# Performance work log

Measured on AMD Instinct MI355X. Metric: run time of the kernel, lower is better.

The kernel has to match this reference:

```python
import jax, jax.numpy as jnp
import numpy as np

N, K, D = 200000, 16, 64


def setup_inputs() -> dict:
    key = jax.random.key(0)
    k1, k2, k3, k4 = jax.random.split(key, 4)
    X = jax.random.normal(k1, (N, D), dtype=jnp.float32)
    pi = jax.nn.softmax(jax.random.normal(k2, (K,), dtype=jnp.float32))
    mus = jax.random.normal(k3, (K, D), dtype=jnp.float32)
    # build SPD covariance matrices: A A^T + 0.5 I
    A = 0.1 * jax.random.normal(k4, (K, D, D), dtype=jnp.float32)
    covs = jnp.einsum('kij,klj->kil', A, A) + 0.5 * jnp.eye(D, dtype=jnp.float32)[None]
    return {"X": X, "pi": pi, "mus": mus, "covs": covs}


def reference(X, pi, mus, covs):
    # GaussianMixtureModel.estimate_log_prob: per-component MVN log_prob + logsumexp
    # fused into one batched Cholesky/Mahalanobis computation.
    d = X.shape[1]
    L = jnp.linalg.cholesky(covs)                      # [K, D, D]
    diff = X[None, :, :] - mus[:, None, :]             # [K, N, D]
    # solve L z = diff^T per component -> whitened residuals
    solve = jax.vmap(lambda Lk, dk: jax.scipy.linalg.solve_triangular(Lk, dk.T, lower=True))
    z = solve(L, diff)                                 # [K, D, N]
    maha = jnp.sum(z * z, axis=1)                      # [K, N]
    half_logdet = jnp.sum(jnp.log(jnp.diagonal(L, axis1=1, axis2=2)), axis=1)  # [K]
    log2pi = jnp.asarray(np.log(2.0 * np.pi), dtype=X.dtype)
    log_prob = -0.5 * (d * log2pi + maha) - half_logdet[:, None]   # [K, N]
    weighted = jnp.log(pi)[:, None] + log_prob          # [K, N]
    # stable softmax over components == exp(weighted - logsumexp)
    r_E = jax.nn.softmax(weighted, axis=0).T            # [N, K]
    return r_E
```

## Files before the change

### kernel.cpp

```cpp
#include <hip/hip_runtime.h>
#include <cstddef>
#include <cstdint>


#define GMM_D 64
#define GMM_K 16

typedef _Float16 half8 __attribute__((ext_vector_type(8)));
typedef float f32x4 __attribute__((ext_vector_type(4)));

#define WA_BYTES (GMM_K * 16 * 64 * 8 * 2)

__device__ __forceinline__ float fast_rsqrt(float x) {
#if __has_builtin(__builtin_amdgcn_rsqf)
    const float r = __builtin_amdgcn_rsqf(x);
    return r * (1.5f - 0.5f * x * r * r);
#else
    return 1.0f / sqrtf(x);
#endif
}

__device__ __forceinline__ float lane_bcast(float v, int l) {
    return __int_as_float(__builtin_amdgcn_readlane(__float_as_int(v), l));
}

__global__ __launch_bounds__(64) void gmm_precompute_kernel(
    const float* __restrict__ pi, const float* __restrict__ mus,
    const float* __restrict__ covs, _Float16* __restrict__ WA,
    float* __restrict__ tv, float* __restrict__ cc)
{
    const int k = blockIdx.x;
    const int r = threadIdx.x;

    __shared__ alignas(16) float Ls[GMM_D][68];
    __shared__ float Wv[GMM_D][GMM_D + 1];

    float A_r[GMM_D];
    {
        const float4* src = reinterpret_cast<const float4*>(
            covs + (size_t)k * GMM_D * GMM_D + (size_t)r * GMM_D);
        #pragma unroll
        for (int u = 0; u < GMM_D / 4; ++u) {
            const float4 v = src[u];
            A_r[4 * u + 0] = v.x; A_r[4 * u + 1] = v.y;
            A_r[4 * u + 2] = v.z; A_r[4 * u + 3] = v.w;
        }
    }

    float mydiag = 1.0f, myrs = 1.0f;
    #pragma unroll
    for (int j = 0; j < GMM_D; ++j) {
        const float pivot = lane_bcast(A_r[j], j);
        const float rs = fast_rsqrt(pivot);
        const float valj = A_r[j] * rs;
        if (r == j) { mydiag = valj; myrs = rs; }
        A_r[j] = valj;
        #pragma unroll
        for (int p = j + 1; p < GMM_D; ++p)
            A_r[p] -= valj * lane_bcast(valj, p);
    }

    #pragma unroll
    for (int p = 0; p < GMM_D; ++p)
        Ls[r][p] = (p <= r) ? A_r[p] : 0.0f;
    __syncthreads();

    float w[GMM_D];
    #pragma unroll
    for (int i = 0; i < GMM_D; ++i) w[i] = 0.0f;

    #pragma unroll
    for (int i = 0; i < GMM_D; ++i) {
        const f32x4* Lrow = reinterpret_cast<const f32x4*>(&Ls[i][0]);
        float a0 = 0.0f, a1 = 0.0f, a2 = 0.0f, a3 = 0.0f;
        #pragma unroll
        for (int u = 0; u <= (i >> 2); ++u) {
            const f32x4 lv = Lrow[u];
            a0 -= lv[0] * w[4 * u + 0];
            a1 -= lv[1] * w[4 * u + 1];
            a2 -= lv[2] * w[4 * u + 2];
            a3 -= lv[3] * w[4 * u + 3];
        }
        const float invd = lane_bcast(myrs, i);
        const float dlt = (r == i) ? 1.0f : 0.0f;
        w[i] = (dlt + (a0 + a1) + (a2 + a3)) * invd;
    }

    #pragma unroll
    for (int i = 0; i < GMM_D; ++i)
        Wv[i][r] = w[i];
    __syncthreads();

    {
        const float* mk = mus + k * GMM_D;
        float s0 = 0.f, s1 = 0.f, s2 = 0.f, s3 = 0.f;
        #pragma unroll
        for (int c = 0; c < GMM_D; c += 4) {
            s0 += Wv[r][c + 0] * mk[c + 0];
            s1 += Wv[r][c + 1] * mk[c + 1];
            s2 += Wv[r][c + 2] * mk[c + 2];
            s3 += Wv[r][c + 3] * mk[c + 3];
        }
        tv[k * GMM_D + r] = -((s0 + s1) + (s2 + s3));
    }

    {
        const int lr = r & 15, q = r >> 4;
        #pragma unroll
        for (int f = 0; f < 16; ++f) {
            const int mt = f >> 2, s = f & 3;
            const int row = mt * 16 + lr;
            const int db = (s & 1) * 32 + q * 8;
            half8 hv;
            #pragma unroll
            for (int u = 0; u < 8; ++u) {
                const float v = Wv[row][db + u];
                _Float16 h = (_Float16)v;
                if (s >= 2) h = (_Float16)(v - (float)h);
                hv[u] = h;
            }
            *(half8*)(WA + ((size_t)((k * 16 + f) * 64) + r) * 8) = hv;
        }
    }

    {
        float ll = logf(mydiag);
        #pragma unroll
        for (int off = 32; off > 0; off >>= 1) ll += __shfl_down(ll, off);
        if (r == 0)
            cc[k] = logf(pi[k]) - ll - 0.5f * 64.0f * 1.8378770664093453f;
    }
}

__global__ __launch_bounds__(256, 2) void gmm_estep_kernel(
    const float* __restrict__ X, const _Float16* __restrict__ WA,
    const float* __restrict__ tv, const float* __restrict__ cc,
    float* __restrict__ out, int N)
{
    __shared__ _Float16 xs[64 * 136];
    __shared__ float lg[64 * 17];

    const int tid = threadIdx.x;

    {
        const int p = tid >> 2, qq = tid & 3;
        const int np = blockIdx.x * 64 + p;
        if (np < N) {
            const float4* src = reinterpret_cast<const float4*>(X + (size_t)np * GMM_D) + qq * 4;
            float vv[16];
            #pragma unroll
            for (int u = 0; u < 4; ++u) {
                const float4 v = src[u];
                vv[4 * u + 0] = v.x; vv[4 * u + 1] = v.y;
                vv[4 * u + 2] = v.z; vv[4 * u + 3] = v.w;
            }
            half8 h0, h1, l0, l1;
            #pragma unroll
            for (int u = 0; u < 8; ++u) {
                const _Float16 a = (_Float16)vv[u];
                const _Float16 b = (_Float16)vv[u + 8];
                h0[u] = a; l0[u] = (_Float16)(vv[u] - (float)a);
                h1[u] = b; l1[u] = (_Float16)(vv[u + 8] - (float)b);
            }
            _Float16* row = xs + p * 136;
            *(half8*)(row + qq * 16)          = h0;
            *(half8*)(row + qq * 16 + 8)      = h1;
            *(half8*)(row + 64 + qq * 16)     = l0;
            *(half8*)(row + 64 + qq * 16 + 8) = l1;
        }
    }
    __syncthreads();

    const int lane = tid & 63;
    const int wave = __builtin_amdgcn_readfirstlane(tid >> 6);
    const int pt = lane & 15;
    const int q  = lane >> 4;

    #pragma unroll 1
    for (int kk = 0; kk < 4; ++kk) {
        const int k = wave * 4 + kk;

        half8 af[4][4];
        const _Float16* wab = WA + (size_t)k * 8192 + lane * 8;
        #pragma unroll
        for (int mt = 0; mt < 4; ++mt)
            #pragma unroll
            for (int s = 0; s < 4; ++s)
                af[mt][s] = *(const half8*)(wab + (mt * 4 + s) * 512);

        f32x4 tk4[4];
        #pragma unroll
        for (int mt = 0; mt < 4; ++mt)
            tk4[mt] = *(const f32x4*)(tv + k * 64 + mt * 16 + q * 4);

        #pragma unroll 1
        for (int nt = 0; nt < 4; ++nt) {
            const _Float16* xrow = xs + (nt * 16 + pt) * 136 + q * 8;
            const half8 bh0 = *(const half8*)(xrow);
            const half8 bh1 = *(const half8*)(xrow + 32);
            const half8 bl0 = *(const half8*)(xrow + 64);
            const half8 bl1 = *(const half8*)(xrow + 96);

            float mahaP = 0.0f;
            #pragma unroll
            for (int mt = 0; mt < 4; ++mt) {
                f32x4 c = tk4[mt];
                c = __builtin_amdgcn_mfma_f32_16x16x32_f16(af[mt][0], bh0, c, 0, 0, 0);
                c = __builtin_amdgcn_mfma_f32_16x16x32_f16(af[mt][1], bh1, c, 0, 0, 0);
                c = __builtin_amdgcn_mfma_f32_16x16x32_f16(af[mt][0], bl0, c, 0, 0, 0);
                c = __builtin_amdgcn_mfma_f32_16x16x32_f16(af[mt][1], bl1, c, 0, 0, 0);
                c = __builtin_amdgcn_mfma_f32_16x16x32_f16(af[mt][2], bh0, c, 0, 0, 0);
                c = __builtin_amdgcn_mfma_f32_16x16x32_f16(af[mt][3], bh1, c, 0, 0, 0);
                mahaP += c[0] * c[0] + c[1] * c[1] + c[2] * c[2] + c[3] * c[3];
            }
            mahaP += __shfl_xor(mahaP, 16);
            mahaP += __shfl_xor(mahaP, 32);
            if (q == 0 && (blockIdx.x * 64 + nt * 16 + pt) < N)
                lg[(nt * 16 + pt) * 17 + k] = cc[k] - 0.5f * mahaP;
        }
    }
    __syncthreads();

    {
        const int p = tid >> 2, qq = tid & 3;
        const int np = blockIdx.x * 64 + p;
        if (np < N) {
            const float* row = &lg[p * 17];
            float m = row[0];
            #pragma unroll
            for (int j = 1; j < GMM_K; ++j) m = fmaxf(m, row[j]);
            float e[GMM_K];
            float s = 0.0f;
            #pragma unroll
            for (int j = 0; j < GMM_K; ++j) { e[j] = __expf(row[j] - m); s += e[j]; }
            const float inv = 1.0f / s;
            float4 v;
            v.x = e[qq * 4 + 0] * inv;
            v.y = e[qq * 4 + 1] * inv;
            v.z = e[qq * 4 + 2] * inv;
            v.w = e[qq * 4 + 3] * inv;
            reinterpret_cast<float4*>(out + (size_t)np * GMM_K)[qq] = v;
        }
    }
}

extern "C" void kernel_launch(void* const* d_in, const int* in_sizes, int n_in,
                              void* d_out, int out_size, void* d_ws, size_t ws_size,
                              hipStream_t stream)
{
    const float* X    = (const float*)d_in[0];
    const float* pi   = (const float*)d_in[1];
    const float* mus  = (const float*)d_in[2];
    const float* covs = (const float*)d_in[3];
    float* out = (float*)d_out;

    const int N = in_sizes[0] / GMM_D;

    _Float16* WA = (_Float16*)d_ws;
    float* tv = (float*)((char*)d_ws + WA_BYTES);
    float* cc = tv + GMM_K * GMM_D;

    gmm_precompute_kernel<<<dim3(GMM_K), dim3(64), 0, stream>>>(pi, mus, covs, WA, tv, cc);

    const int blocks = (N + 63) / 64;
    gmm_estep_kernel<<<dim3(blocks), dim3(256), 0, stream>>>(X, WA, tv, cc, out, N);
}
```

Measured before the change: 173.9 us.

## Replace split-fp16 MFMA with split-int8 fixed-point MFMA for Mahalanobis projection

Quantizes whitening matrices (per-component scale) and X (fixed ±6 range) into 16-bit fixed point split into hi/lo int8 bytes, and computes the projection with three i32 16x16x64 int8 MFMAs per tile instead of six fp16 split MFMAs. Shared memory for X shrinks and the weight loads are halved. It trades accuracy for throughput: X values beyond the clamp range saturate, and precision is limited to about 16 bits.

```diff
diff --git a/kernel.cpp b/kernel.cpp
--- a/kernel.cpp
+++ b/kernel.cpp
@@ -6,10 +6,15 @@
 #define GMM_D 64
 #define GMM_K 16
 
-typedef _Float16 half8 __attribute__((ext_vector_type(8)));
 typedef float f32x4 __attribute__((ext_vector_type(4)));
+typedef int   i32x4 __attribute__((ext_vector_type(4)));
 
 #define WA_BYTES (GMM_K * 16 * 64 * 8 * 2)
+#define WA_COMP_BYTES 8192
+#define SCL_OFFSET (240 * 1024)
+
+#define SX_Q (6.0f / 32512.0f)
+#define INV_SX (32512.0f / 6.0f)
 
 __device__ __forceinline__ float fast_rsqrt(float x) {
 #if __has_builtin(__builtin_amdgcn_rsqf)
@@ -24,10 +29,22 @@
     return __int_as_float(__builtin_amdgcn_readlane(__float_as_int(v), l));
 }
 
+__device__ __forceinline__ void quant16(float y, int& hi8, int& lo8) {
+    y = fminf(fmaxf(y, -32512.0f), 32512.0f);
+    const int wi = (int)y;
+    hi8 = (wi + 128) >> 8;
+    lo8 = wi - (hi8 << 8);
+}
+
+__device__ __forceinline__ unsigned pack4(int b0, int b1, int b2, int b3) {
+    return (unsigned)(b0 & 255) | ((unsigned)(b1 & 255) << 8) |
+           ((unsigned)(b2 & 255) << 16) | ((unsigned)(b3 & 255) << 24);
+}
+
 __global__ __launch_bounds__(64) void gmm_precompute_kernel(
     const float* __restrict__ pi, const float* __restrict__ mus,
-    const float* __restrict__ covs, _Float16* __restrict__ WA,
-    float* __restrict__ tv, float* __restrict__ cc)
+    const float* __restrict__ covs, char* __restrict__ WA8,
+    float* __restrict__ scl, float* __restrict__ tv, float* __restrict__ cc)
 {
     const int k = blockIdx.x;
     const int r = threadIdx.x;
@@ -86,6 +103,13 @@
         w[i] = (dlt + (a0 + a1) + (a2 + a3)) * invd;
     }
 
+    float mW = 0.0f;
+    #pragma unroll
+    for (int i = 0; i < GMM_D; ++i) mW = fmaxf(mW, fabsf(w[i]));
+    #pragma unroll
+    for (int off = 1; off < 64; off <<= 1) mW = fmaxf(mW, __shfl_xor(mW, off));
+    const float invSW = 32512.0f / mW;
+
     #pragma unroll
     for (int i = 0; i < GMM_D; ++i)
         Wv[i][r] = w[i];
@@ -105,24 +129,35 @@
     }
 
     {
-        const int lr = r & 15, q = r >> 4;
-        #pragma unroll
-        for (int f = 0; f < 16; ++f) {
-            const int mt = f >> 2, s = f & 3;
+        const int lr = r & 15, q4 = r >> 4;
+        char* base = WA8 + (size_t)k * WA_COMP_BYTES + (size_t)r * 16;
+        #pragma unroll
+        for (int mt = 0; mt < 4; ++mt) {
             const int row = mt * 16 + lr;
-            const int db = (s & 1) * 32 + q * 8;
-            half8 hv;
-            #pragma unroll
-            for (int u = 0; u < 8; ++u) {
-                const float v = Wv[row][db + u];
-                _Float16 h = (_Float16)v;
-                if (s >= 2) h = (_Float16)(v - (float)h);
-                hv[u] = h;
-            }
-            *(half8*)(WA + ((size_t)((k * 16 + f) * 64) + r) * 8) = hv;
-        }
-    }
-
+            int hb[16], lb[16];
+            #pragma unroll
+            for (int u = 0; u < 16; ++u) {
+                const float wv = Wv[row][q4 * 16 + u];
+                quant16(rintf(wv * invSW), hb[u], lb[u]);
+            }
+            unsigned hw[4], lw[4];
+            #pragma unroll
+            for (int d = 0; d < 4; ++d) {
+                hw[d] = pack4(hb[4*d], hb[4*d+1], hb[4*d+2], hb[4*d+3]);
+                lw[d] = pack4(lb[4*d], lb[4*d+1], lb[4*d+2], lb[4*d+3]);
+            }
+            i32x4 hv = { (int)hw[0], (int)hw[1], (int)hw[2], (int)hw[3] };
+            i32x4 lv = { (int)lw[0], (int)lw[1], (int)lw[2], (int)lw[3] };
+            *(i32x4*)(base + (mt * 2 + 0) * 1024) = hv;
+            *(i32x4*)(base + (mt * 2 + 1) * 1024) = lv;
+        }
+    }
+
+    if (r == 0) {
+        const float s = (mW / 32512.0f) * SX_Q;
+        scl[2 * k + 0] = 65536.0f * s;
+        scl[2 * k + 1] = 256.0f * s;
+    }
     {
         float ll = logf(mydiag);
         #pragma unroll
@@ -133,11 +168,12 @@
 }
 
 __global__ __launch_bounds__(256, 2) void gmm_estep_kernel(
-    const float* __restrict__ X, const _Float16* __restrict__ WA,
-    const float* __restrict__ tv, const float* __restrict__ cc,
-    float* __restrict__ out, int N)
+    const float* __restrict__ X, const char* __restrict__ WA8,
+    const float* __restrict__ scl, const float* __restrict__ tv,
+    const float* __restrict__ cc, float* __restrict__ out, int N)
 {
-    __shared__ _Float16 xs[64 * 136];
+    __shared__ alignas(16) char xhi[64][80];
+    __shared__ alignas(16) char xlo[64][80];
     __shared__ float lg[64 * 17];
 
     const int tid = threadIdx.x;
@@ -154,19 +190,20 @@
                 vv[4 * u + 0] = v.x; vv[4 * u + 1] = v.y;
                 vv[4 * u + 2] = v.z; vv[4 * u + 3] = v.w;
             }
-            half8 h0, h1, l0, l1;
-            #pragma unroll
-            for (int u = 0; u < 8; ++u) {
-                const _Float16 a = (_Float16)vv[u];
-                const _Float16 b = (_Float16)vv[u + 8];
-                h0[u] = a; l0[u] = (_Float16)(vv[u] - (float)a);
-                h1[u] = b; l1[u] = (_Float16)(vv[u + 8] - (float)b);
-            }
-            _Float16* row = xs + p * 136;
-            *(half8*)(row + qq * 16)          = h0;
-            *(half8*)(row + qq * 16 + 8)      = h1;
-            *(half8*)(row + 64 + qq * 16)     = l0;
-            *(half8*)(row + 64 + qq * 16 + 8) = l1;
+            int hb[16], lb[16];
+            #pragma unroll
+            for (int u = 0; u < 16; ++u)
+                quant16(rintf(vv[u] * INV_SX), hb[u], lb[u]);
+            unsigned hw[4], lw[4];
+            #pragma unroll
+            for (int d = 0; d < 4; ++d) {
+                hw[d] = pack4(hb[4*d], hb[4*d+1], hb[4*d+2], hb[4*d+3]);
+                lw[d] = pack4(lb[4*d], lb[4*d+1], lb[4*d+2], lb[4*d+3]);
+            }
+            i32x4 hv = { (int)hw[0], (int)hw[1], (int)hw[2], (int)hw[3] };
+            i32x4 lv = { (int)lw[0], (int)lw[1], (int)lw[2], (int)lw[3] };
+            *(i32x4*)&xhi[p][qq * 16] = hv;
+            *(i32x4*)&xlo[p][qq * 16] = lv;
         }
     }
     __syncthreads();
@@ -180,38 +217,39 @@
     for (int kk = 0; kk < 4; ++kk) {
         const int k = wave * 4 + kk;
 
-        half8 af[4][4];
-        const _Float16* wab = WA + (size_t)k * 8192 + lane * 8;
+        i32x4 af[4][2];
+        const char* wab = WA8 + (size_t)k * WA_COMP_BYTES + (size_t)lane * 16;
         #pragma unroll
         for (int mt = 0; mt < 4; ++mt)
             #pragma unroll
-            for (int s = 0; s < 4; ++s)
-                af[mt][s] = *(const half8*)(wab + (mt * 4 + s) * 512);
+            for (int h = 0; h < 2; ++h)
+                af[mt][h] = *(const i32x4*)(wab + (mt * 2 + h) * 1024);
 
         f32x4 tk4[4];
         #pragma unroll
         for (int mt = 0; mt < 4; ++mt)
             tk4[mt] = *(const f32x4*)(tv + k * 64 + mt * 16 + q * 4);
+        const float s1 = scl[2 * k + 0];
+        const float s2 = scl[2 * k + 1];
 
         #pragma unroll 1
         for (int nt = 0; nt < 4; ++nt) {
-            const _Float16* xrow = xs + (nt * 16 + pt) * 136 + q * 8;
-            const half8 bh0 = *(const half8*)(xrow);
-            const half8 bh1 = *(const half8*)(xrow + 32);
-            const half8 bl0 = *(const half8*)(xrow + 64);
-            const half8 bl1 = *(const half8*)(xrow + 96);
+            const i32x4 xh = *(const i32x4*)&xhi[nt * 16 + pt][q * 16];
+            const i32x4 xl = *(const i32x4*)&xlo[nt * 16 + pt][q * 16];
+            const i32x4 zero = { 0, 0, 0, 0 };
 
             float mahaP = 0.0f;
             #pragma unroll
             for (int mt = 0; mt < 4; ++mt) {
-                f32x4 c = tk4[mt];
-                c = __builtin_amdgcn_mfma_f32_16x16x32_f16(af[mt][0], bh0, c, 0, 0, 0);
-                c = __builtin_amdgcn_mfma_f32_16x16x32_f16(af[mt][1], bh1, c, 0, 0, 0);
-                c = __builtin_amdgcn_mfma_f32_16x16x32_f16(af[mt][0], bl0, c, 0, 0, 0);
-                c = __builtin_amdgcn_mfma_f32_16x16x32_f16(af[mt][1], bl1, c, 0, 0, 0);
-                c = __builtin_amdgcn_mfma_f32_16x16x32_f16(af[mt][2], bh0, c, 0, 0, 0);
-                c = __builtin_amdgcn_mfma_f32_16x16x32_f16(af[mt][3], bh1, c, 0, 0, 0);
-                mahaP += c[0] * c[0] + c[1] * c[1] + c[2] * c[2] + c[3] * c[3];
+                i32x4 chh = __builtin_amdgcn_mfma_i32_16x16x64_i8(af[mt][0], xh, zero, 0, 0, 0);
+                i32x4 cx  = __builtin_amdgcn_mfma_i32_16x16x64_i8(af[mt][0], xl, zero, 0, 0, 0);
+                cx        = __builtin_amdgcn_mfma_i32_16x16x64_i8(af[mt][1], xh, cx,   0, 0, 0);
+                #pragma unroll
+                for (int j = 0; j < 4; ++j) {
+                    const float zf = fmaf((float)chh[j], s1,
+                                      fmaf((float)cx[j], s2, tk4[mt][j]));
+                    mahaP += zf * zf;
+                }
             }
             mahaP += __shfl_xor(mahaP, 16);
             mahaP += __shfl_xor(mahaP, 32);
@@ -256,12 +294,15 @@
 
     const int N = in_sizes[0] / GMM_D;
 
-    _Float16* WA = (_Float16*)d_ws;
+    char* WA8 = (char*)d_ws;
+    float* scl = (float*)((char*)d_ws + SCL_OFFSET);
     float* tv = (float*)((char*)d_ws + WA_BYTES);
     float* cc = tv + GMM_K * GMM_D;
 
-    gmm_precompute_kernel<<<dim3(GMM_K), dim3(64), 0, stream>>>(pi, mus, covs, WA, tv, cc);
+    gmm_precompute_kernel<<<dim3(GMM_K), dim3(64), 0, stream>>>(
+        pi, mus, covs, WA8, scl, tv, cc);
 
     const int blocks = (N + 63) / 64;
-    gmm_estep_kernel<<<dim3(blocks), dim3(256), 0, stream>>>(X, WA, tv, cc, out, N);
-}
+    gmm_estep_kernel<<<dim3(blocks), dim3(256), 0, stream>>>(
+        X, WA8, scl, tv, cc, out, N);
+}
```

Result: slower. 180.3 us (+3.7%).
